# Kernel tuning notes

Hardware: AMD Instinct MI355X
Metric: run time of the kernel (lower is better)

The kernel has to match this reference:

```python
import jax, jax.numpy as jnp
import numpy as np

# norse default LIFParameters
DT = 1e-3
TAU_SYN_INV = 200.0
TAU_MEM_INV = 100.0
V_LEAK = 0.0
V_TH = 1.0
V_RESET = 0.0


def heaviside(x):
    return (x > 0).astype(x.dtype)


def setup_inputs() -> dict:
    key = jax.random.key(0)
    ks = jax.random.split(key, 5)
    T, B, I, H, O = 14, 4096, 2048, 1024, 128
    x = (jax.random.uniform(ks[0], (T, B, I), dtype=jnp.float32) < 0.2).astype(jnp.float32)  # spike train
    w_in = jax.random.normal(ks[1], (H, I), dtype=jnp.float32) * (1.0 / np.sqrt(I))
    w_rec = jax.random.normal(ks[2], (H, H), dtype=jnp.float32) * (1.0 / np.sqrt(H))
    out_w = jax.random.normal(ks[3], (O, H), dtype=jnp.float32) * (1.0 / np.sqrt(H))
    out_b = jax.random.normal(ks[4], (O,), dtype=jnp.float32) * 0.01
    return {"x": x, "w_in": w_in, "w_rec": w_rec, "out_w": out_w, "out_b": out_b}


def reference(x, w_in, w_rec, out_w, out_b):
    T, B, _ = x.shape
    H = w_in.shape[0]
    z0 = jnp.zeros((B, H), dtype=x.dtype)
    v0 = jnp.full((B, H), V_LEAK, dtype=x.dtype)
    i0 = jnp.zeros((B, H), dtype=x.dtype)

    def step(carry, x_t):
        z, v, i = carry
        v_dec = v + DT * TAU_MEM_INV * ((V_LEAK - v) + i)   # membrane integration
        i_dec = i - DT * TAU_SYN_INV * i                    # synaptic decay
        z_new = heaviside(v_dec - V_TH)                     # spike
        v_new = (1.0 - z_new) * v_dec + z_new * V_RESET     # reset
        i_new = i_dec + x_t @ w_in.T + z @ w_rec.T          # input + recurrent current
        return (z_new, v_new, i_new), None

    (z_T, _, _), _ = jax.lax.scan(step, (z0, v0, i0), x)
    return z_T @ out_w.T + out_b
```

## Files before the change

kernel.cpp:

```cpp
#include <hip/hip_runtime.h>
#include <stdint.h>

#define T_STEPS 14
#define B_DIM   4096
#define I_DIM   2048
#define H_DIM   1024
#define O_DIM   128
#define K_TOT   3072
#define ZBYTES  ((size_t)B_DIM * H_DIM)

#define WSCALE_F 33554432.0f

typedef __bf16  bf16x8  __attribute__((ext_vector_type(8)));
typedef float   floatx4 __attribute__((ext_vector_type(4)));
typedef int     int4v   __attribute__((ext_vector_type(4)));
typedef int     int16v  __attribute__((ext_vector_type(16)));
typedef unsigned long long u64;

__device__ __forceinline__ uint16_t f2bf_rne(float f) {
    uint32_t u = __float_as_uint(f);
    u += 0x7fffu + ((u >> 16) & 1u);
    return (uint16_t)(u >> 16);
}
__device__ __forceinline__ float bf2f(uint16_t h) {
    return __uint_as_float(((uint32_t)h) << 16);
}

__device__ __forceinline__ void gload_lds16(const void* g, void* l) {
    __builtin_amdgcn_global_load_lds((__attribute__((address_space(1))) void*)g,
                                     (__attribute__((address_space(3))) void*)l, 16, 0, 0);
}


__global__ void split_w_kernel(const float* __restrict__ w_in, const float* __restrict__ w_rec,
                               int8_t* __restrict__ WB) {
    int idx = blockIdx.x * 256 + threadIdx.x;
    int h = idx / K_TOT;
    int k = idx - h * K_TOT;
    float w = (k < I_DIM) ? w_in[(size_t)h * I_DIM + k]
                          : w_rec[(size_t)h * H_DIM + (k - I_DIM)];
    int W  = __float2int_rn(w * WSCALE_F);
    int d0 = (int8_t)(W & 0xFF);
    int r1 = (W - d0) >> 8;
    int d1 = (int8_t)(r1 & 0xFF);
    int d2 = (r1 - d1) >> 8;
    int nt = h >> 5, n32 = h & 31;
    int ktw = k >> 7, k128 = k & 127;
    int kk = k128 >> 5, half = (k128 >> 4) & 1, j = k128 & 15;
    int lane = half * 32 + n32;
    size_t base = (size_t)(nt * 24 + ktw) * 12288 + kk * 1024 + lane * 16 + j;
    WB[base] = (int8_t)d0; WB[base + 4096] = (int8_t)d1; WB[base + 8192] = (int8_t)d2;
}

__global__ void split_ow_kernel(const float* __restrict__ out_w, uint16_t* __restrict__ OW3) {
    int idx = blockIdx.x * 256 + threadIdx.x;
    float w = out_w[idx];
    uint16_t hi = f2bf_rne(w);
    float r1 = w - bf2f(hi);
    uint16_t mid = f2bf_rne(r1);
    float r2 = r1 - bf2f(mid);
    uint16_t lo = f2bf_rne(r2);
    const size_t S = (size_t)O_DIM * H_DIM;
    OW3[idx] = hi; OW3[idx + S] = mid; OW3[idx + 2 * S] = lo;
}

__global__ void cvt_x_kernel(const float* __restrict__ x, int8_t* __restrict__ xb) {
    size_t gid = (size_t)blockIdx.x * 256 + threadIdx.x;
    int g = (int)(gid & 1023);
    size_t chunk = gid >> 10;
    int kt   = (int)(chunk & 15);
    int mIdx = (int)((chunk >> 4) & 31);
    int t    = (int)(chunk >> 9);
    int group = g >> 8, kk = (g >> 6) & 3, lane = g & 63;
    int half = lane >> 5, row32 = lane & 31;
    int b = mIdx * 128 + group * 32 + row32;
    int k = kt * 128 + kk * 32 + half * 16;
    const float4* src = (const float4*)(x + ((size_t)t * B_DIM + b) * I_DIM + k);
    union { int8_t bytes[16]; int4v v; } u;
#pragma unroll
    for (int q = 0; q < 4; ++q) {
        float4 f = src[q];
        u.bytes[q * 4 + 0] = (int8_t)(f.x > 0.5f);
        u.bytes[q * 4 + 1] = (int8_t)(f.y > 0.5f);
        u.bytes[q * 4 + 2] = (int8_t)(f.z > 0.5f);
        u.bytes[q * 4 + 3] = (int8_t)(f.w > 0.5f);
    }
    ((int4v*)xb)[gid] = u.v;
}

__global__ void zero_cnt_kernel(uint32_t* __restrict__ cnt) {
    __hip_atomic_store(&cnt[blockIdx.x * 256 + threadIdx.x], 0u,
                       __ATOMIC_RELAXED, __HIP_MEMORY_SCOPE_AGENT);
}

__device__ __forceinline__ void loadA(const int8_t* __restrict__ aP, int4v (&a)[4]) {
    a[0] = *(const int4v*)(aP);
    a[1] = *(const int4v*)(aP + 1024);
    a[2] = *(const int4v*)(aP + 2048);
    a[3] = *(const int4v*)(aP + 3072);
}

__device__ __forceinline__ void stage_b(const int8_t* __restrict__ bA,
                                        const int8_t* __restrict__ bB,
                                        int8_t* dst, int wave, int lane) {
    gload_lds16(bA + (size_t)wave * 1024 + lane * 16,       dst + wave * 1024);
    gload_lds16(bA + (size_t)(4 + wave) * 1024 + lane * 16, dst + (4 + wave) * 1024);
    gload_lds16(bA + (size_t)(8 + wave) * 1024 + lane * 16, dst + (8 + wave) * 1024);
    gload_lds16(bB + (size_t)wave * 1024 + lane * 16,       dst + 12288 + wave * 1024);
    gload_lds16(bB + (size_t)(4 + wave) * 1024 + lane * 16, dst + 12288 + (4 + wave) * 1024);
    gload_lds16(bB + (size_t)(8 + wave) * 1024 + lane * 16, dst + 12288 + (8 + wave) * 1024);
}

__device__ __forceinline__ void lif_iter(const int8_t* __restrict__ aPn,
                                         const int8_t* __restrict__ bPnA,
                                         const int8_t* __restrict__ bPnB,
                                         const int8_t* cur, int8_t* nxt,
                                         int4v (&aA)[4],
                                         int wave, int lane, bool stage_next,
                                         int16v (&acc)[2][3]) {
    if (stage_next) {
        stage_b(bPnA, bPnB, nxt, wave, lane);
        __builtin_amdgcn_sched_barrier(0);
        asm volatile("s_waitcnt vmcnt(6)" ::: "memory");
    } else {
        asm volatile("s_waitcnt vmcnt(0)" ::: "memory");
    }
    __builtin_amdgcn_s_barrier();
    __builtin_amdgcn_sched_barrier(0);
    __builtin_amdgcn_s_setprio(1);
#pragma unroll
    for (int kk = 0; kk < 4; ++kk) {
#pragma unroll
        for (int n = 0; n < 2; ++n) {
#pragma unroll
            for (int s = 0; s < 3; ++s) {
                int4v bF = *(const int4v*)(cur + n * 12288 + s * 4096 + kk * 1024 + lane * 16);
                acc[n][s] = __builtin_amdgcn_mfma_i32_32x32x32_i8(aA[kk], bF, acc[n][s], 0, 0, 0);
            }
        }
    }
    __builtin_amdgcn_s_setprio(0);
    __builtin_amdgcn_sched_barrier(0);
    if (aPn) loadA(aPn, aA);
    asm volatile("s_waitcnt lgkmcnt(0)" ::: "memory");
    __builtin_amdgcn_s_barrier();
}

template<int NKT>
__device__ __forceinline__ void run_phase(const int8_t* __restrict__ aW,
                                          const int8_t* __restrict__ bA,
                                          const int8_t* __restrict__ bB,
                                          int8_t* sB0, int8_t* sB1,
                                          int4v (&aA)[4],
                                          int wave, int lane, int16v (&acc)[2][3]) {
#pragma unroll 1
    for (int kt = 0; kt + 2 < NKT; kt += 2) {
        lif_iter(aW + (size_t)(kt + 1) * 16384, bA + (size_t)(kt + 1) * 12288,
                 bB + (size_t)(kt + 1) * 12288, sB0, sB1, aA, wave, lane, true, acc);
        lif_iter(aW + (size_t)(kt + 2) * 16384, bA + (size_t)(kt + 2) * 12288,
                 bB + (size_t)(kt + 2) * 12288, sB1, sB0, aA, wave, lane, true, acc);
    }
    lif_iter(aW + (size_t)(NKT - 1) * 16384, bA + (size_t)(NKT - 1) * 12288,
             bB + (size_t)(NKT - 1) * 12288, sB0, sB1, aA, wave, lane, true, acc);
    lif_iter(nullptr, nullptr, nullptr, sB1, sB0, aA, wave, lane, false, acc);
}

__launch_bounds__(256, 2)
__global__ void lif_persist_kernel(const int8_t* __restrict__ Xall,
                                   const int8_t* __restrict__ WB,
                                   int8_t* __restrict__ ZS,
                                   uint16_t* __restrict__ Zbf,
                                   uint32_t* __restrict__ cnt) {
    __shared__ int8_t sB0[24576];
    __shared__ int8_t sB1[24576];
    __shared__ int8_t sZ[8192];

    const int tid  = threadIdx.x;
    const int wave = tid >> 6, lane = tid & 63;
    const int lane32 = lane & 31, hl = lane >> 5;

    const int bid = blockIdx.x;
    const int xs = bid & 7, q = bid >> 3;
    const int mIdx = xs * 4 + (q & 3);
    const int nt2  = q >> 2;

    const int mBase = mIdx * 128, nBase = nt2 * 64;
    const int8_t* wbA = WB + (size_t)(2 * nt2) * 24 * 12288;
    const int8_t* wbB = WB + (size_t)(2 * nt2 + 1) * 24 * 12288;
    const int fragOff = wave * 4096 + lane * 16;

    float vmem[2][16], isyn[2][16];
#pragma unroll
    for (int n = 0; n < 2; ++n)
#pragma unroll
        for (int r = 0; r < 16; ++r) { vmem[n][r] = 0.0f; isyn[n][r] = 0.0f; }

    int4v aA[4];

    stage_b(wbA, wbB, sB0, wave, lane);
    loadA(Xall + (size_t)mIdx * 16 * 16384 + fragOff, aA);

    for (int t = 0; t < T_STEPS; ++t) {
        int16v acc[2][3] = {};

        const int8_t* XtW = Xall + (size_t)t * ((size_t)B_DIM * I_DIM)
                          + (size_t)mIdx * 16 * 16384 + fragOff;
        run_phase<16>(XtW, wbA, wbB, sB0, sB1, aA, wave, lane, acc);

        if (t > 0) {
            const int8_t* zbA = wbA + (size_t)16 * 12288;
            const int8_t* zbB = wbB + (size_t)16 * 12288;
            stage_b(zbA, zbB, sB0, wave, lane);
            if (tid == 0) {
                const uint32_t* f = cnt + ((size_t)mIdx * 13 + (t - 1)) * 32;
                while (__hip_atomic_load((uint32_t*)f, __ATOMIC_RELAXED, __HIP_MEMORY_SCOPE_AGENT) < 16u)
                    __builtin_amdgcn_s_sleep(2);
            }
            __syncthreads();
            const int8_t* zW = ZS + (size_t)(t - 1) * ZBYTES + (size_t)mIdx * 8 * 16384 + fragOff;
            loadA(zW, aA);
            run_phase<8>(zW, zbA, zbB, sB0, sB1, aA, wave, lane, acc);
        }

        if (t + 1 < T_STEPS) {
            stage_b(wbA, wbB, sB0, wave, lane);
            loadA(Xall + (size_t)(t + 1) * ((size_t)B_DIM * I_DIM)
                  + (size_t)mIdx * 16 * 16384 + fragOff, aA);
        }

#pragma unroll
        for (int n = 0; n < 2; ++n) {
#pragma unroll
            for (int r = 0; r < 16; ++r) {
#pragma clang fp contract(off)
                float cur = (float)acc[n][2][r] * (1.0f / 512.0f)
                          + (float)acc[n][1][r] * (1.0f / 131072.0f)
                          + (float)acc[n][0][r] * (1.0f / 33554432.0f);
                int row = (r & 3) + 8 * (r >> 2) + 4 * hl;
                float v_dec = vmem[n][r] + 0.1f * ((0.0f - vmem[n][r]) + isyn[n][r]);
                float i_dec = isyn[n][r] - 0.2f * isyn[n][r];
                bool z = (v_dec > 1.0f);
                vmem[n][r] = z ? 0.0f : v_dec;
                isyn[n][r] = i_dec + cur;
                if (t == T_STEPS - 1) {
                    int b = mBase + wave * 32 + row;
                    int h = nBase + n * 32 + lane32;
                    Zbf[(size_t)b * H_DIM + h] = z ? (uint16_t)0x3F80 : (uint16_t)0;
                } else {
                    sZ[n * 4096 + wave * 1024 + ((lane32 >> 4) * 32 + row) * 16 + (lane32 & 15)]
                        = z ? (int8_t)1 : (int8_t)0;
                }
            }
        }

        if (t < T_STEPS - 1) {
            __syncthreads();
#pragma unroll
            for (int n = 0; n < 2; ++n) {
                const u64* sp = (const u64*)&sZ[n * 4096 + tid * 16];
                u64 v0 = sp[0], v1 = sp[1];
                const int ntn = nt2 * 2 + n;
                int8_t* dst = ZS + (size_t)t * ZBYTES + ((size_t)mIdx * 8 + (ntn >> 2)) * 16384
                            + (tid >> 6) * 4096 + (ntn & 3) * 1024 + (tid & 63) * 16;
                __hip_atomic_store((u64*)dst,       v0, __ATOMIC_RELAXED, __HIP_MEMORY_SCOPE_AGENT);
                __hip_atomic_store((u64*)(dst + 8), v1, __ATOMIC_RELAXED, __HIP_MEMORY_SCOPE_AGENT);
            }
            __syncthreads();
            if (tid == 0)
                __hip_atomic_fetch_add(&cnt[((size_t)mIdx * 13 + t) * 32], 1u,
                                       __ATOMIC_RELAXED, __HIP_MEMORY_SCOPE_AGENT);
        }
    }
}

__launch_bounds__(256)
__global__ void out_gemm_kernel(const uint16_t* __restrict__ Zfin,
                                const uint16_t* __restrict__ OW3,
                                const float* __restrict__ out_b,
                                float* __restrict__ out) {
    __shared__ uint16_t sA[16 * 32];
    __shared__ uint16_t sB[3][128 * 32];

    const int tid  = threadIdx.x;
    const int wave = tid >> 6, lane = tid & 63;
    const int quad = lane >> 4, col = lane & 15;

    const int mBase = blockIdx.x * 16;

    floatx4 acc[2] = {};

    const int ldRow = lane >> 2;
    const int ldCol = (lane & 3) * 8;

    for (int kt = 0; kt < H_DIM / 32; ++kt) {
        const int kb = kt * 32;
        __syncthreads();
        if (wave == 0) {
            const uint16_t* g = Zfin + (size_t)(mBase + ldRow) * H_DIM + kb + ldCol;
            gload_lds16(g, &sA[0]);
        }
#pragma unroll
        for (int s = 0; s < 3; ++s) {
            const uint16_t* wsrc = OW3 + (size_t)s * O_DIM * H_DIM;
#pragma unroll
            for (int j = 0; j < 2; ++j) {
                const int rseg = j * 4 + wave;
                const uint16_t* g = wsrc + (size_t)(rseg * 16 + ldRow) * H_DIM + kb + ldCol;
                gload_lds16(g, &sB[s][rseg * 16 * 32]);
            }
        }
        __syncthreads();

        bf16x8 aF = *reinterpret_cast<const bf16x8*>(&sA[col * 32 + quad * 8]);
#pragma unroll
        for (int s = 0; s < 3; ++s) {
#pragma unroll
            for (int ni = 0; ni < 2; ++ni) {
                int row = wave * 32 + ni * 16 + col;
                bf16x8 bF = *reinterpret_cast<const bf16x8*>(&sB[s][row * 32 + quad * 8]);
                acc[ni] = __builtin_amdgcn_mfma_f32_16x16x32_bf16(aF, bF, acc[ni], 0, 0, 0);
            }
        }
    }

    {
#pragma clang fp contract(off)
#pragma unroll
        for (int ni = 0; ni < 2; ++ni)
#pragma unroll
            for (int r = 0; r < 4; ++r) {
                int b = mBase + quad * 4 + r;
                int h = wave * 32 + ni * 16 + col;
                out[(size_t)b * O_DIM + h] = acc[ni][r] + out_b[h];
            }
    }
}

extern "C" void kernel_launch(void* const* d_in, const int* in_sizes, int n_in,
                              void* d_out, int out_size, void* d_ws, size_t ws_size,
                              hipStream_t stream) {
    const float* x     = (const float*)d_in[0];
    const float* w_in  = (const float*)d_in[1];
    const float* w_rec = (const float*)d_in[2];
    const float* out_w = (const float*)d_in[3];
    const float* out_b = (const float*)d_in[4];
    float* out = (float*)d_out;

    char* ws = (char*)d_ws;
    size_t off = 0;
    int8_t*   WB   = (int8_t*)(ws + off);   off += (size_t)3 * H_DIM * K_TOT;
    uint16_t* OW3  = (uint16_t*)(ws + off); off += (size_t)3 * O_DIM * H_DIM * 2;
    int8_t*   Xall = (int8_t*)(ws + off);   off += (size_t)T_STEPS * B_DIM * I_DIM;
    uint16_t* Zbf  = (uint16_t*)(ws + off); off += (size_t)B_DIM * H_DIM * 2;
    int8_t*   ZS   = (int8_t*)(ws + off);   off += (size_t)13 * ZBYTES;
    uint32_t* CNT  = (uint32_t*)(ws + off); off += (size_t)32 * 13 * 32 * 4;

    split_w_kernel<<<(H_DIM * K_TOT) / 256, 256, 0, stream>>>(w_in, w_rec, WB);
    split_ow_kernel<<<(O_DIM * H_DIM) / 256, 256, 0, stream>>>(out_w, OW3);
    cvt_x_kernel<<<(int)(((size_t)T_STEPS * B_DIM * I_DIM / 16) / 256), 256, 0, stream>>>(x, Xall);
    zero_cnt_kernel<<<(32 * 13 * 32) / 256, 256, 0, stream>>>(CNT);

    lif_persist_kernel<<<dim3(512), dim3(256), 0, stream>>>(Xall, WB, ZS, Zbf, CNT);

    out_gemm_kernel<<<B_DIM / 16, 256, 0, stream>>>(Zbf, OW3, out_b, out);
}
```

Before: 1.254 ms.

## Stage A operand tiles through double-buffered LDS via direct global-to-LDS loads

The A-operand fragments (spike inputs and previous-step spikes) were loaded straight into registers after each k-step's MFMAs. They are now staged asynchronously into double-buffered LDS with gload_lds16, alongside the B tiles, and read back from LDS before the MFMAs. The goal is to hide the A global-load latency behind compute the same way B already is. The cost is shared memory growing to 80 KB per block, which, if it still holds, keeps two blocks per CU, plus extra LDS reads. The sZ buffer is now aliased onto sA1.

```diff
diff --git a/kernel.cpp b/kernel.cpp
--- a/kernel.cpp
+++ b/kernel.cpp
@@ -93,13 +93,14 @@
                        __ATOMIC_RELAXED, __HIP_MEMORY_SCOPE_AGENT);
 }
 
-__device__ __forceinline__ void loadA(const int8_t* __restrict__ aP, int4v (&a)[4]) {
-    a[0] = *(const int4v*)(aP);
-    a[1] = *(const int4v*)(aP + 1024);
-    a[2] = *(const int4v*)(aP + 2048);
-    a[3] = *(const int4v*)(aP + 3072);
-}
-
+__device__ __forceinline__ void stage_a(const int8_t* __restrict__ aC, int8_t* dst,
+                                        int wave, int lane) {
+#pragma unroll
+    for (int j = 0; j < 4; ++j) {
+        const int seg = j * 4 + wave;
+        gload_lds16(aC + (size_t)seg * 1024 + lane * 16, dst + seg * 1024);
+    }
+}
 __device__ __forceinline__ void stage_b(const int8_t* __restrict__ bA,
                                         const int8_t* __restrict__ bB,
                                         int8_t* dst, int wave, int lane) {
@@ -111,22 +112,27 @@
     gload_lds16(bB + (size_t)(8 + wave) * 1024 + lane * 16, dst + 12288 + (8 + wave) * 1024);
 }
 
-__device__ __forceinline__ void lif_iter(const int8_t* __restrict__ aPn,
-                                         const int8_t* __restrict__ bPnA,
-                                         const int8_t* __restrict__ bPnB,
-                                         const int8_t* cur, int8_t* nxt,
-                                         int4v (&aA)[4],
+__device__ __forceinline__ void lif_iter(const int8_t* __restrict__ aCn,
+                                         const int8_t* __restrict__ bAn,
+                                         const int8_t* __restrict__ bBn,
+                                         const int8_t* curA, const int8_t* curB,
+                                         int8_t* nxtA, int8_t* nxtB,
                                          int wave, int lane, bool stage_next,
                                          int16v (&acc)[2][3]) {
     if (stage_next) {
-        stage_b(bPnA, bPnB, nxt, wave, lane);
+        stage_a(aCn, nxtA, wave, lane);
+        stage_b(bAn, bBn, nxtB, wave, lane);
         __builtin_amdgcn_sched_barrier(0);
-        asm volatile("s_waitcnt vmcnt(6)" ::: "memory");
+        asm volatile("s_waitcnt vmcnt(10)" ::: "memory");
     } else {
         asm volatile("s_waitcnt vmcnt(0)" ::: "memory");
     }
     __builtin_amdgcn_s_barrier();
     __builtin_amdgcn_sched_barrier(0);
+    int4v aF[4];
+#pragma unroll
+    for (int kk = 0; kk < 4; ++kk)
+        aF[kk] = *(const int4v*)(curA + wave * 4096 + kk * 1024 + lane * 16);
     __builtin_amdgcn_s_setprio(1);
 #pragma unroll
     for (int kk = 0; kk < 4; ++kk) {
@@ -134,35 +140,32 @@
         for (int n = 0; n < 2; ++n) {
 #pragma unroll
             for (int s = 0; s < 3; ++s) {
-                int4v bF = *(const int4v*)(cur + n * 12288 + s * 4096 + kk * 1024 + lane * 16);
-                acc[n][s] = __builtin_amdgcn_mfma_i32_32x32x32_i8(aA[kk], bF, acc[n][s], 0, 0, 0);
+                int4v bF = *(const int4v*)(curB + n * 12288 + s * 4096 + kk * 1024 + lane * 16);
+                acc[n][s] = __builtin_amdgcn_mfma_i32_32x32x32_i8(aF[kk], bF, acc[n][s], 0, 0, 0);
             }
         }
     }
     __builtin_amdgcn_s_setprio(0);
-    __builtin_amdgcn_sched_barrier(0);
-    if (aPn) loadA(aPn, aA);
     asm volatile("s_waitcnt lgkmcnt(0)" ::: "memory");
     __builtin_amdgcn_s_barrier();
 }
 
 template<int NKT>
-__device__ __forceinline__ void run_phase(const int8_t* __restrict__ aW,
+__device__ __forceinline__ void run_phase(const int8_t* __restrict__ aC,
                                           const int8_t* __restrict__ bA,
                                           const int8_t* __restrict__ bB,
-                                          int8_t* sB0, int8_t* sB1,
-                                          int4v (&aA)[4],
+                                          int8_t* sA0, int8_t* sA1, int8_t* sB0, int8_t* sB1,
                                           int wave, int lane, int16v (&acc)[2][3]) {
 #pragma unroll 1
     for (int kt = 0; kt + 2 < NKT; kt += 2) {
-        lif_iter(aW + (size_t)(kt + 1) * 16384, bA + (size_t)(kt + 1) * 12288,
-                 bB + (size_t)(kt + 1) * 12288, sB0, sB1, aA, wave, lane, true, acc);
-        lif_iter(aW + (size_t)(kt + 2) * 16384, bA + (size_t)(kt + 2) * 12288,
-                 bB + (size_t)(kt + 2) * 12288, sB1, sB0, aA, wave, lane, true, acc);
-    }
-    lif_iter(aW + (size_t)(NKT - 1) * 16384, bA + (size_t)(NKT - 1) * 12288,
-             bB + (size_t)(NKT - 1) * 12288, sB0, sB1, aA, wave, lane, true, acc);
-    lif_iter(nullptr, nullptr, nullptr, sB1, sB0, aA, wave, lane, false, acc);
+        lif_iter(aC + (size_t)(kt + 1) * 16384, bA + (size_t)(kt + 1) * 12288,
+                 bB + (size_t)(kt + 1) * 12288, sA0, sB0, sA1, sB1, wave, lane, true, acc);
+        lif_iter(aC + (size_t)(kt + 2) * 16384, bA + (size_t)(kt + 2) * 12288,
+                 bB + (size_t)(kt + 2) * 12288, sA1, sB1, sA0, sB0, wave, lane, true, acc);
+    }
+    lif_iter(aC + (size_t)(NKT - 1) * 16384, bA + (size_t)(NKT - 1) * 12288,
+             bB + (size_t)(NKT - 1) * 12288, sA0, sB0, sA1, sB1, wave, lane, true, acc);
+    lif_iter(nullptr, nullptr, nullptr, sA1, sB1, sA0, sB0, wave, lane, false, acc);
 }
 
 __launch_bounds__(256, 2)
@@ -171,9 +174,12 @@
                                    int8_t* __restrict__ ZS,
                                    uint16_t* __restrict__ Zbf,
                                    uint32_t* __restrict__ cnt) {
-    __shared__ int8_t sB0[24576];
-    __shared__ int8_t sB1[24576];
-    __shared__ int8_t sZ[8192];
+    __shared__ int8_t sMem[81920];
+    int8_t* const sA0 = sMem;
+    int8_t* const sA1 = sMem + 16384;
+    int8_t* const sB0 = sMem + 32768;
+    int8_t* const sB1 = sMem + 57344;
+    int8_t* const sZ  = sA1;
 
     const int tid  = threadIdx.x;
     const int wave = tid >> 6, lane = tid & 63;
@@ -187,7 +193,6 @@
     const int mBase = mIdx * 128, nBase = nt2 * 64;
     const int8_t* wbA = WB + (size_t)(2 * nt2) * 24 * 12288;
     const int8_t* wbB = WB + (size_t)(2 * nt2 + 1) * 24 * 12288;
-    const int fragOff = wave * 4096 + lane * 16;
 
     float vmem[2][16], isyn[2][16];
 #pragma unroll
@@ -195,17 +200,15 @@
 #pragma unroll
         for (int r = 0; r < 16; ++r) { vmem[n][r] = 0.0f; isyn[n][r] = 0.0f; }
 
-    int4v aA[4];
-
+    stage_a(Xall + (size_t)mIdx * 16 * 16384, sA0, wave, lane);
     stage_b(wbA, wbB, sB0, wave, lane);
-    loadA(Xall + (size_t)mIdx * 16 * 16384 + fragOff, aA);
 
     for (int t = 0; t < T_STEPS; ++t) {
         int16v acc[2][3] = {};
 
-        const int8_t* XtW = Xall + (size_t)t * ((size_t)B_DIM * I_DIM)
-                          + (size_t)mIdx * 16 * 16384 + fragOff;
-        run_phase<16>(XtW, wbA, wbB, sB0, sB1, aA, wave, lane, acc);
+        const int8_t* XtC = Xall + (size_t)t * ((size_t)B_DIM * I_DIM)
+                          + (size_t)mIdx * 16 * 16384;
+        run_phase<16>(XtC, wbA, wbB, sA0, sA1, sB0, sB1, wave, lane, acc);
 
         if (t > 0) {
             const int8_t* zbA = wbA + (size_t)16 * 12288;
@@ -217,15 +220,15 @@
                     __builtin_amdgcn_s_sleep(2);
             }
             __syncthreads();
-            const int8_t* zW = ZS + (size_t)(t - 1) * ZBYTES + (size_t)mIdx * 8 * 16384 + fragOff;
-            loadA(zW, aA);
-            run_phase<8>(zW, zbA, zbB, sB0, sB1, aA, wave, lane, acc);
+            const int8_t* zC = ZS + (size_t)(t - 1) * ZBYTES + (size_t)mIdx * 8 * 16384;
+            stage_a(zC, sA0, wave, lane);
+            run_phase<8>(zC, zbA, zbB, sA0, sA1, sB0, sB1, wave, lane, acc);
         }
 
         if (t + 1 < T_STEPS) {
+            stage_a(Xall + (size_t)(t + 1) * ((size_t)B_DIM * I_DIM)
+                    + (size_t)mIdx * 16 * 16384, sA0, wave, lane);
             stage_b(wbA, wbB, sB0, wave, lane);
-            loadA(Xall + (size_t)(t + 1) * ((size_t)B_DIM * I_DIM)
-                  + (size_t)mIdx * 16 * 16384 + fragOff, aA);
         }
 
 #pragma unroll
```

After: 1.213 ms. 1.03x faster.
